# Kernel tuning notes

Hardware: AMD Instinct MI355X
Metric: run time of the kernel (lower is better)

Reference implementation:

```python
import jax, jax.numpy as jnp
import numpy as np

N = 8192      # agent_num
F = 128       # feature dim
P = 16        # persona dim
E = 262144    # edges (N * avg_degree 32)


def setup_inputs() -> dict:
    key = jax.random.key(0)
    ks = jax.random.split(key, 10)
    return {
        "feature": jax.random.normal(ks[0], (N, F), dtype=jnp.float32),
        "next_feature": jax.random.normal(ks[1], (N, F), dtype=jnp.float32),
        "persona_t": jax.random.uniform(ks[2], (N, P), dtype=jnp.float32),
        "alpha": jax.random.normal(ks[3], (P,), dtype=jnp.float32),
        "beta": jax.random.normal(ks[4], (P,), dtype=jnp.float32),
        "gamma": jax.random.normal(ks[5], (P,), dtype=jnp.float32),
        "act_src": jax.random.randint(ks[6], (E,), 0, N, dtype=jnp.int32),
        "act_dst": jax.random.randint(ks[7], (E,), 0, N, dtype=jnp.int32),
        "edge_src": jax.random.randint(ks[8], (E,), 0, N, dtype=jnp.int32),
        "edge_dst": jax.random.randint(ks[9], (E,), 0, N, dtype=jnp.int32),
    }


def _row_l2_normalize(x):
    # norm_func: divide each row by its L2 norm (scatter-add of squares in torch)
    norms = jnp.sqrt(jnp.sum(x * x, axis=1, keepdims=True))
    return x / norms


def reference(feature, next_feature, persona_t, alpha, beta, gamma,
              act_src, act_dst, edge_src, edge_dst):
    n, f = feature.shape

    # ---- impact (gamma) path: adj_sim_self(next_action, old - new) ----
    diff = feature - next_feature                           # [N, F]
    # hadamard(adj, diff @ diff.T): only dot products on action edges
    impact_vals = jnp.sum(diff[act_src] * diff[act_dst], axis=1) / f   # [E]
    gamma_row = persona_t @ gamma                            # [N] persona-weighted gamma
    reward_impact = impact_vals * gamma_row[act_src]         # row-wise multiply

    # ---- similarity (alpha) path: adj_sim(next_action, norm(next_feature)) ----
    # step() normalizes next_feature, then adj_sim normalizes again (idempotent)
    nf = _row_l2_normalize(_row_l2_normalize(next_feature))  # [N, F]
    sim_vals = jnp.sum(nf[act_src] * nf[act_dst], axis=1)    # [E] cosine sims on edges
    alpha_row = persona_t @ alpha                            # [N]
    reward_sim = sim_vals * alpha_row[act_src]

    # ---- cost (beta) path: old edges (binary) * persona_beta broadcast over rows ----
    beta_row = persona_t @ beta                              # [N]
    reward_cost = beta_row[edge_src]                         # [E] (edge value = 1)

    # ---- reward = reward_sim - reward_cost + reward_impact on the union of supports ----
    reward = jnp.zeros((n, n), dtype=feature.dtype)
    reward = reward.at[act_src, act_dst].add(reward_sim + reward_impact)
    reward = reward.at[edge_src, edge_dst].add(-reward_cost)
    return reward
```

## Files before the change

kernel.cpp:

```cpp
#include <hip/hip_runtime.h>
#include <hip/hip_fp16.h>

#define N_AGENTS 8192
#define FDIM 128
#define PDIM 16
#define NEDGES 262144
#define CAP 128
#define OVERCAP 4096

typedef float floatx4 __attribute__((ext_vector_type(4)));

__global__ __launch_bounds__(256) void row_prep_k(
        const float* __restrict__ feature,
        const float* __restrict__ next_feature,
        const float* __restrict__ persona,
        const float* __restrict__ alpha,
        const float* __restrict__ beta,
        const float* __restrict__ gamma,
        __half2* __restrict__ T2,
        float2* __restrict__ scale,
        float* __restrict__ brow,
        int* __restrict__ cntA,
        int* __restrict__ cntC,
        int* __restrict__ ocnt) {
    int row  = (blockIdx.x * blockDim.x + threadIdx.x) >> 6;
    int lane = threadIdx.x & 63;
    if (blockIdx.x == 0 && threadIdx.x == 0) *ocnt = 0;
    if (row >= N_AGENTS) return;

    const float2* f2 = (const float2*)(feature      + (size_t)row * FDIM);
    const float2* n2 = (const float2*)(next_feature + (size_t)row * FDIM);
    float2 f  = f2[lane];
    float2 nx = n2[lane];

    float2 d = make_float2(f.x - nx.x, f.y - nx.y);
    float ss = nx.x * nx.x + nx.y * nx.y;

    float pa = 0.f, pb = 0.f, pg = 0.f;
    if (lane < PDIM) {
        float p = persona[(size_t)row * PDIM + lane];
        pa = p * alpha[lane];
        pb = p * beta[lane];
        pg = p * gamma[lane];
    }

    #pragma unroll
    for (int off = 32; off > 0; off >>= 1) {
        ss += __shfl_xor(ss, off);
        pa += __shfl_xor(pa, off);
        pb += __shfl_xor(pb, off);
        pg += __shfl_xor(pg, off);
    }

    float inv = 1.0f / sqrtf(ss);
    __half2* trow = T2 + (size_t)row * 128;
    trow[lane]      = __float22half2_rn(make_float2(nx.x * inv, nx.y * inv));
    trow[64 + lane] = __float22half2_rn(d);

    if (lane == 0) {
        scale[row] = make_float2(pa, pg * (1.0f / FDIM));
        brow[row]  = pb;
        cntA[row]  = 0;
        cntC[row]  = 0;
    }
}

__device__ inline float dot8(float4 a, float4 b) {
    const __half2* ha = (const __half2*)&a;
    const __half2* hb = (const __half2*)&b;
    float s = 0.f;
    #pragma unroll
    for (int j = 0; j < 4; ++j) {
        float2 fa = __half22float2(ha[j]);
        float2 fb = __half22float2(hb[j]);
        s += fa.x * fb.x + fa.y * fb.y;
    }
    return s;
}

__global__ __launch_bounds__(256) void edge_bin_k(
        const int* __restrict__ asrc,
        const int* __restrict__ adst,
        const int* __restrict__ esrc,
        const int* __restrict__ edst,
        int* __restrict__ cntA,
        int* __restrict__ cntC,
        int* __restrict__ binsA,
        int* __restrict__ binsC,
        int* __restrict__ ocnt,
        int4* __restrict__ olist) {
    int t = blockIdx.x * 256 + threadIdx.x;
    if (t < NEDGES) {
        int s = asrc[t];
        int d = adst[t];
        int pos = atomicAdd(&cntA[s], 1);
        if (pos < CAP) binsA[(size_t)s * CAP + pos] = d;
        else { int op = atomicAdd(ocnt, 1); if (op < OVERCAP) olist[op] = make_int4(s, d, 0, 0); }
    } else {
        int e = t - NEDGES;
        int s = esrc[e];
        int d = edst[e];
        int pos = atomicAdd(&cntC[s], 1);
        if (pos < CAP) binsC[(size_t)s * CAP + pos] = d;
        else { int op = atomicAdd(ocnt, 1); if (op < OVERCAP) olist[op] = make_int4(s, d, 1, 0); }
    }
}

__global__ __launch_bounds__(256) void row_assemble_k(
        const int* __restrict__ cntA,
        const int* __restrict__ binsA,
        const int* __restrict__ cntC,
        const int* __restrict__ binsC,
        const __half* __restrict__ T,
        const float2* __restrict__ scale,
        const float* __restrict__ brow,
        float* __restrict__ out) {
    __shared__ float rowbuf[N_AGENTS];
    int r   = blockIdx.x;
    int tid = threadIdx.x;

    floatx4* rb4 = (floatx4*)rowbuf;
    floatx4 z = (floatx4)0.f;
    #pragma unroll
    for (int i = 0; i < 8; ++i)
        rb4[tid + i * 256] = z;

    int grp    = tid >> 4;
    int lane16 = tid & 15;
    int i0     = lane16 * 2;
    const float4* tr = (const float4*)(T + (size_t)r * 256);
    float4 tsA = tr[i0];
    float4 tsB = tr[i0 + 1];
    float2 sc  = scale[r];
    float  br  = brow[r];
    int cA = cntA[r]; cA = cA < CAP ? cA : CAP;
    int cC = cntC[r]; cC = cC < CAP ? cC : CAP;
    __syncthreads();

    for (int i = grp; i < cA; i += 16) {
        int d = binsA[(size_t)r * CAP + i];
        const float4* td = (const float4*)(T + (size_t)d * 256);
        float acc = dot8(tsA, td[i0]) + dot8(tsB, td[i0 + 1]);
        acc += __shfl_xor(acc, 1, 16);
        acc += __shfl_xor(acc, 2, 16);
        acc += __shfl_xor(acc, 4, 16);
        float other = __shfl_xor(acc, 8, 16);
        if (lane16 == 0)
            atomicAdd(&rowbuf[d], acc * sc.x + other * sc.y);
    }
    for (int i = tid; i < cC; i += 256)
        atomicAdd(&rowbuf[binsC[(size_t)r * CAP + i]], -br);
    __syncthreads();

    floatx4* dst = (floatx4*)(out + (size_t)r * N_AGENTS);
    #pragma unroll
    for (int i = 0; i < 8; ++i)
        __builtin_nontemporal_store(rb4[tid + i * 256], &dst[tid + i * 256]);
}

__global__ __launch_bounds__(256) void overflow_k(
        const int* __restrict__ ocnt,
        const int4* __restrict__ olist,
        const __half* __restrict__ T,
        const float2* __restrict__ scale,
        const float* __restrict__ brow,
        float* __restrict__ out) {
    int n = *ocnt;
    n = n < OVERCAP ? n : OVERCAP;
    int grp    = threadIdx.x >> 4;
    int lane16 = threadIdx.x & 15;
    int i0     = lane16 * 2;
    for (int i = grp; i < n; i += 16) {
        int4 rec = olist[i];
        if (rec.z) {
            if (lane16 == 0)
                atomicAdd(out + (size_t)rec.x * N_AGENTS + rec.y, -brow[rec.x]);
        } else {
            const float4* ts = (const float4*)(T + (size_t)rec.x * 256);
            const float4* td = (const float4*)(T + (size_t)rec.y * 256);
            float acc = dot8(ts[i0], td[i0]) + dot8(ts[i0 + 1], td[i0 + 1]);
            acc += __shfl_xor(acc, 1, 16);
            acc += __shfl_xor(acc, 2, 16);
            acc += __shfl_xor(acc, 4, 16);
            float other = __shfl_xor(acc, 8, 16);
            if (lane16 == 0) {
                float2 sc = scale[rec.x];
                atomicAdd(out + (size_t)rec.x * N_AGENTS + rec.y,
                          acc * sc.x + other * sc.y);
            }
        }
    }
}

extern "C" void kernel_launch(void* const* d_in, const int* in_sizes, int n_in,
                              void* d_out, int out_size, void* d_ws, size_t ws_size,
                              hipStream_t stream) {
    const float* feature      = (const float*)d_in[0];
    const float* next_feature = (const float*)d_in[1];
    const float* persona      = (const float*)d_in[2];
    const float* alpha        = (const float*)d_in[3];
    const float* beta         = (const float*)d_in[4];
    const float* gamma        = (const float*)d_in[5];
    const int*   act_src      = (const int*)d_in[6];
    const int*   act_dst      = (const int*)d_in[7];
    const int*   edge_src     = (const int*)d_in[8];
    const int*   edge_dst     = (const int*)d_in[9];

    float* out = (float*)d_out;

    char* ws = (char*)d_ws;
    __half* T     = (__half*)ws;   ws += (size_t)N_AGENTS * 256 * sizeof(__half);
    float2* scale = (float2*)ws;   ws += (size_t)N_AGENTS * sizeof(float2);
    float*  brow  = (float*)ws;    ws += (size_t)N_AGENTS * sizeof(float);
    int*    cntA  = (int*)ws;      ws += (size_t)N_AGENTS * sizeof(int);
    int*    cntC  = (int*)ws;      ws += (size_t)N_AGENTS * sizeof(int);
    int*    binsA = (int*)ws;      ws += (size_t)N_AGENTS * CAP * sizeof(int);
    int*    binsC = (int*)ws;      ws += (size_t)N_AGENTS * CAP * sizeof(int);
    int*    ocnt  = (int*)ws;      ws += 16;
    int4*   olist = (int4*)ws;

    row_prep_k<<<N_AGENTS / 4, 256, 0, stream>>>(
        feature, next_feature, persona, alpha, beta, gamma,
        (__half2*)T, scale, brow, cntA, cntC, ocnt);

    edge_bin_k<<<(2 * NEDGES) / 256, 256, 0, stream>>>(
        act_src, act_dst, edge_src, edge_dst,
        cntA, cntC, binsA, binsC, ocnt, olist);

    row_assemble_k<<<N_AGENTS, 256, 0, stream>>>(
        cntA, binsA, cntC, binsC, T, scale, brow, out);

    overflow_k<<<1, 256, 0, stream>>>(ocnt, olist, T, scale, brow, out);
}
```

Measured before the change: 331.6 us.

## Fuse row prep with edge binning and fold overflow handling into assembly

Row preparation and edge binning now run as one launch with interleaved blocks, and the counters are zeroed by a memset. The separate overflow kernel is removed: each row block scans the overflow list and applies any entries for its own row into the shared row buffer. This cuts launch count and the serial single-block overflow pass. The cost is an extra memset and an overflow-list scan in every row block, which is normally empty.

```diff
diff --git a/kernel.cpp b/kernel.cpp
--- a/kernel.cpp
+++ b/kernel.cpp
@@ -10,7 +10,22 @@
 
 typedef float floatx4 __attribute__((ext_vector_type(4)));
 
-__global__ __launch_bounds__(256) void row_prep_k(
+__device__ inline float dot8(float4 a, float4 b) {
+    const __half2* ha = (const __half2*)&a;
+    const __half2* hb = (const __half2*)&b;
+    float s = 0.f;
+    #pragma unroll
+    for (int j = 0; j < 4; ++j) {
+        float2 fa = __half22float2(ha[j]);
+        float2 fb = __half22float2(hb[j]);
+        s += fa.x * fb.x + fa.y * fb.y;
+    }
+    return s;
+}
+
+#define PREP_BLOCKS (N_AGENTS / 4)
+#define BIN_BLOCKS  ((2 * NEDGES) / 256)
+__global__ __launch_bounds__(256) void prep_bin_k(
         const float* __restrict__ feature,
         const float* __restrict__ next_feature,
         const float* __restrict__ persona,
@@ -20,65 +35,6 @@
         __half2* __restrict__ T2,
         float2* __restrict__ scale,
         float* __restrict__ brow,
-        int* __restrict__ cntA,
-        int* __restrict__ cntC,
-        int* __restrict__ ocnt) {
-    int row  = (blockIdx.x * blockDim.x + threadIdx.x) >> 6;
-    int lane = threadIdx.x & 63;
-    if (blockIdx.x == 0 && threadIdx.x == 0) *ocnt = 0;
-    if (row >= N_AGENTS) return;
-
-    const float2* f2 = (const float2*)(feature      + (size_t)row * FDIM);
-    const float2* n2 = (const float2*)(next_feature + (size_t)row * FDIM);
-    float2 f  = f2[lane];
-    float2 nx = n2[lane];
-
-    float2 d = make_float2(f.x - nx.x, f.y - nx.y);
-    float ss = nx.x * nx.x + nx.y * nx.y;
-
-    float pa = 0.f, pb = 0.f, pg = 0.f;
-    if (lane < PDIM) {
-        float p = persona[(size_t)row * PDIM + lane];
-        pa = p * alpha[lane];
-        pb = p * beta[lane];
-        pg = p * gamma[lane];
-    }
-
-    #pragma unroll
-    for (int off = 32; off > 0; off >>= 1) {
-        ss += __shfl_xor(ss, off);
-        pa += __shfl_xor(pa, off);
-        pb += __shfl_xor(pb, off);
-        pg += __shfl_xor(pg, off);
-    }
-
-    float inv = 1.0f / sqrtf(ss);
-    __half2* trow = T2 + (size_t)row * 128;
-    trow[lane]      = __float22half2_rn(make_float2(nx.x * inv, nx.y * inv));
-    trow[64 + lane] = __float22half2_rn(d);
-
-    if (lane == 0) {
-        scale[row] = make_float2(pa, pg * (1.0f / FDIM));
-        brow[row]  = pb;
-        cntA[row]  = 0;
-        cntC[row]  = 0;
-    }
-}
-
-__device__ inline float dot8(float4 a, float4 b) {
-    const __half2* ha = (const __half2*)&a;
-    const __half2* hb = (const __half2*)&b;
-    float s = 0.f;
-    #pragma unroll
-    for (int j = 0; j < 4; ++j) {
-        float2 fa = __half22float2(ha[j]);
-        float2 fb = __half22float2(hb[j]);
-        s += fa.x * fb.x + fa.y * fb.y;
-    }
-    return s;
-}
-
-__global__ __launch_bounds__(256) void edge_bin_k(
         const int* __restrict__ asrc,
         const int* __restrict__ adst,
         const int* __restrict__ esrc,
@@ -89,20 +45,60 @@
         int* __restrict__ binsC,
         int* __restrict__ ocnt,
         int4* __restrict__ olist) {
-    int t = blockIdx.x * 256 + threadIdx.x;
-    if (t < NEDGES) {
-        int s = asrc[t];
-        int d = adst[t];
-        int pos = atomicAdd(&cntA[s], 1);
-        if (pos < CAP) binsA[(size_t)s * CAP + pos] = d;
-        else { int op = atomicAdd(ocnt, 1); if (op < OVERCAP) olist[op] = make_int4(s, d, 0, 0); }
+    int bid = blockIdx.x >> 1;
+    if ((blockIdx.x & 1) == 0) {
+        int row  = bid * 4 + (threadIdx.x >> 6);
+        int lane = threadIdx.x & 63;
+
+        const float2* f2 = (const float2*)(feature      + (size_t)row * FDIM);
+        const float2* n2 = (const float2*)(next_feature + (size_t)row * FDIM);
+        float2 f  = f2[lane];
+        float2 nx = n2[lane];
+
+        float2 d = make_float2(f.x - nx.x, f.y - nx.y);
+        float ss = nx.x * nx.x + nx.y * nx.y;
+
+        float pa = 0.f, pb = 0.f, pg = 0.f;
+        if (lane < PDIM) {
+            float p = persona[(size_t)row * PDIM + lane];
+            pa = p * alpha[lane];
+            pb = p * beta[lane];
+            pg = p * gamma[lane];
+        }
+
+        #pragma unroll
+        for (int off = 32; off > 0; off >>= 1) {
+            ss += __shfl_xor(ss, off);
+            pa += __shfl_xor(pa, off);
+            pb += __shfl_xor(pb, off);
+            pg += __shfl_xor(pg, off);
+        }
+
+        float inv = 1.0f / sqrtf(ss);
+        __half2* trow = T2 + (size_t)row * 128;
+        trow[lane]      = __float22half2_rn(make_float2(nx.x * inv, nx.y * inv));
+        trow[64 + lane] = __float22half2_rn(d);
+
+        if (lane == 0) {
+            scale[row] = make_float2(pa, pg * (1.0f / FDIM));
+            brow[row]  = pb;
+        }
     } else {
-        int e = t - NEDGES;
-        int s = esrc[e];
-        int d = edst[e];
-        int pos = atomicAdd(&cntC[s], 1);
-        if (pos < CAP) binsC[(size_t)s * CAP + pos] = d;
-        else { int op = atomicAdd(ocnt, 1); if (op < OVERCAP) olist[op] = make_int4(s, d, 1, 0); }
+        int t = bid * 256 + threadIdx.x;
+        if (t < NEDGES) {
+            int s = asrc[t];
+            int d = adst[t];
+            int pos = atomicAdd(&cntA[s], 1);
+            if (pos < CAP) binsA[(size_t)s * CAP + pos] = d;
+            else { int op = atomicAdd(ocnt, 1); if (op < OVERCAP) olist[op] = make_int4(s, d, 0, 0); }
+        } else {
+            int e = t - NEDGES;
+            int s = esrc[e];
+            int d = edst[e];
+            int pos = atomicAdd(&cntC[s], 1);
+            if (pos < CAP) binsC[(size_t)s * CAP + pos] = d;
+            else { int op = atomicAdd(ocnt, 1); if (op < OVERCAP) olist[op] = make_int4(s, d, 1, 0); }
+        }
     }
 }
 
@@ -114,6 +110,8 @@
         const __half* __restrict__ T,
         const float2* __restrict__ scale,
         const float* __restrict__ brow,
+        const int* __restrict__ ocnt,
+        const int4* __restrict__ olist,
         float* __restrict__ out) {
     __shared__ float rowbuf[N_AGENTS];
     int r   = blockIdx.x;
@@ -135,6 +133,8 @@
     float  br  = brow[r];
     int cA = cntA[r]; cA = cA < CAP ? cA : CAP;
     int cC = cntC[r]; cC = cC < CAP ? cC : CAP;
+    int nov = *ocnt;
+    nov = nov < OVERCAP ? nov : OVERCAP;
     __syncthreads();
 
     for (int i = grp; i < cA; i += 16) {
@@ -150,46 +150,31 @@
     }
     for (int i = tid; i < cC; i += 256)
         atomicAdd(&rowbuf[binsC[(size_t)r * CAP + i]], -br);
+
+    if (nov > 0) {
+        for (int i = grp; i < nov; i += 16) {
+            int4 rec = olist[i];
+            if (rec.x != r) continue;
+            if (rec.z) {
+                if (lane16 == 0) atomicAdd(&rowbuf[rec.y], -br);
+            } else {
+                const float4* td = (const float4*)(T + (size_t)rec.y * 256);
+                float acc = dot8(tsA, td[i0]) + dot8(tsB, td[i0 + 1]);
+                acc += __shfl_xor(acc, 1, 16);
+                acc += __shfl_xor(acc, 2, 16);
+                acc += __shfl_xor(acc, 4, 16);
+                float other = __shfl_xor(acc, 8, 16);
+                if (lane16 == 0)
+                    atomicAdd(&rowbuf[rec.y], acc * sc.x + other * sc.y);
+            }
+        }
+    }
     __syncthreads();
 
     floatx4* dst = (floatx4*)(out + (size_t)r * N_AGENTS);
     #pragma unroll
     for (int i = 0; i < 8; ++i)
         __builtin_nontemporal_store(rb4[tid + i * 256], &dst[tid + i * 256]);
-}
-
-__global__ __launch_bounds__(256) void overflow_k(
-        const int* __restrict__ ocnt,
-        const int4* __restrict__ olist,
-        const __half* __restrict__ T,
-        const float2* __restrict__ scale,
-        const float* __restrict__ brow,
-        float* __restrict__ out) {
-    int n = *ocnt;
-    n = n < OVERCAP ? n : OVERCAP;
-    int grp    = threadIdx.x >> 4;
-    int lane16 = threadIdx.x & 15;
-    int i0     = lane16 * 2;
-    for (int i = grp; i < n; i += 16) {
-        int4 rec = olist[i];
-        if (rec.z) {
-            if (lane16 == 0)
-                atomicAdd(out + (size_t)rec.x * N_AGENTS + rec.y, -brow[rec.x]);
-        } else {
-            const float4* ts = (const float4*)(T + (size_t)rec.x * 256);
-            const float4* td = (const float4*)(T + (size_t)rec.y * 256);
-            float acc = dot8(ts[i0], td[i0]) + dot8(ts[i0 + 1], td[i0 + 1]);
-            acc += __shfl_xor(acc, 1, 16);
-            acc += __shfl_xor(acc, 2, 16);
-            acc += __shfl_xor(acc, 4, 16);
-            float other = __shfl_xor(acc, 8, 16);
-            if (lane16 == 0) {
-                float2 sc = scale[rec.x];
-                atomicAdd(out + (size_t)rec.x * N_AGENTS + rec.y,
-                          acc * sc.x + other * sc.y);
-            }
-        }
-    }
 }
 
 extern "C" void kernel_launch(void* const* d_in, const int* in_sizes, int n_in,
@@ -214,21 +199,19 @@
     float*  brow  = (float*)ws;    ws += (size_t)N_AGENTS * sizeof(float);
     int*    cntA  = (int*)ws;      ws += (size_t)N_AGENTS * sizeof(int);
     int*    cntC  = (int*)ws;      ws += (size_t)N_AGENTS * sizeof(int);
+    int*    ocnt  = (int*)ws;      ws += 16;
     int*    binsA = (int*)ws;      ws += (size_t)N_AGENTS * CAP * sizeof(int);
     int*    binsC = (int*)ws;      ws += (size_t)N_AGENTS * CAP * sizeof(int);
-    int*    ocnt  = (int*)ws;      ws += 16;
     int4*   olist = (int4*)ws;
 
-    row_prep_k<<<N_AGENTS / 4, 256, 0, stream>>>(
+    hipMemsetAsync(cntA, 0, 2 * (size_t)N_AGENTS * sizeof(int) + 16, stream);
+
+    prep_bin_k<<<PREP_BLOCKS + BIN_BLOCKS, 256, 0, stream>>>(
         feature, next_feature, persona, alpha, beta, gamma,
-        (__half2*)T, scale, brow, cntA, cntC, ocnt);
-
-    edge_bin_k<<<(2 * NEDGES) / 256, 256, 0, stream>>>(
+        (__half2*)T, scale, brow,
         act_src, act_dst, edge_src, edge_dst,
         cntA, cntC, binsA, binsC, ocnt, olist);
 
     row_assemble_k<<<N_AGENTS, 256, 0, stream>>>(
-        cntA, binsA, cntC, binsC, T, scale, brow, out);
-
-    overflow_k<<<1, 256, 0, stream>>>(ocnt, olist, T, scale, brow, out);
-}
+        cntA, binsA, cntC, binsC, T, scale, brow, ocnt, olist, out);
+}
```

Result: no change. 328.9 us (-0.8%).
